# Kernel tuning notes

Measured on AMD Instinct MI355X. Metric: run time of the kernel, lower is better.

The kernel has to match this reference:

```python
import jax, jax.numpy as jnp
import numpy as np

B, S, D = 8, 2048, 768
N_SPANS = 512
MAX_W = 30  # static max span width (inclusive width in tokens)
H = 100
NEG = -1e30


def setup_inputs() -> dict:
    key = jax.random.key(0)
    k1, k2, k3, k4, k5, k6 = jax.random.split(key, 6)
    seq_tensor = jax.random.normal(k1, (B, S, D), dtype=jnp.float32)
    starts = jax.random.randint(k2, (B, N_SPANS), 0, S - MAX_W)
    widths = jax.random.randint(k3, (B, N_SPANS), 1, MAX_W + 1)  # span length in [1, MAX_W]
    ends_excl = starts + widths  # exclusive end, as module expects
    span_indices = jnp.stack([starts, ends_excl], axis=-1).astype(jnp.int64)
    span_mask = (jax.random.uniform(k4, (B, N_SPANS)) > 0.1).astype(jnp.int32)
    att_w = jax.random.normal(k5, (D, 1), dtype=jnp.float32) / np.sqrt(D)
    att_b = jnp.zeros((1,), dtype=jnp.float32)
    ffnn_w = jax.random.normal(k6, (D, H), dtype=jnp.float32) / np.sqrt(D)
    ffnn_b = jnp.zeros((H,), dtype=jnp.float32)
    return {"seq_tensor": seq_tensor, "span_indices": span_indices, "span_mask": span_mask,
            "att_w": att_w, "att_b": att_b, "ffnn_w": ffnn_w, "ffnn_b": ffnn_b}


def reference(seq_tensor, span_indices, span_mask, att_w, att_b, ffnn_w, ffnn_b):
    # exclusive end -> inclusive end (span_end_is_exclusive=True)
    starts = span_indices[..., 0]
    ends = span_indices[..., 1] - 1
    widths = ends - starts  # inclusive width - 1, in [0, MAX_W-1]

    offsets = jnp.arange(MAX_W)  # [W]
    raw_idx = starts[..., None] + offsets  # [B, N, W]
    width_mask = offsets <= widths[..., None]  # [B, N, W]
    idx = jnp.where(width_mask, raw_idx, 0)

    # global attention logits over the sequence: [B, S]
    att_logits = (jnp.einsum('bsd,do->bso', seq_tensor, att_w) + att_b)[..., 0]

    # gather span token embeddings and logits: [B, N, W, D], [B, N, W]
    span_emb = jax.vmap(lambda seq, i: seq[i])(seq_tensor, idx)
    span_logits = jax.vmap(lambda lg, i: lg[i])(att_logits, idx)

    # masked softmax over span width
    span_logits = jnp.where(width_mask, span_logits, NEG)
    attn = jax.nn.softmax(span_logits, axis=-1)  # [B, N, W]

    attended = jnp.einsum('bnw,bnwd->bnd', attn, span_emb)  # [B, N, D]
    attended = attended * span_mask.astype(attended.dtype)[..., None]

    # FeedForward: 1 layer Linear + tanh (dropout=0)
    out = jnp.tanh(jnp.einsum('bnd,dh->bnh', attended, ffnn_w) + ffnn_b)
    return out
```

## Files before the change

### kernel.cpp

```cpp
#include <hip/hip_runtime.h>
#include <cstdint>
#include <cstddef>

#define NB 8
#define NS 2048
#define ND 768
#define NSP 512
#define MAXW 30
#define NH 100
#define LDP 104
#define NKS 24
#define NCF 8
#define BM 16
#define NIT 12

typedef __attribute__((ext_vector_type(8))) short short8;
typedef __attribute__((ext_vector_type(4))) float floatx4;

union U4S8 { uint4 v; short8 s8; unsigned u[4]; unsigned short us[8]; };

__device__ inline unsigned short f2bf(float f) {
    unsigned u = __float_as_uint(f);
    return (unsigned short)((u + 0x7fffu + ((u >> 16) & 1u)) >> 16);
}

__device__ inline void split2(float x0, float x1, unsigned& hi, unsigned& lo) {
    unsigned u0 = __float_as_uint(x0), u1 = __float_as_uint(x1);
    unsigned h0 = u0 & 0xFFFF0000u, h1 = u1 & 0xFFFF0000u;
    hi = (u0 >> 16) | h1;
    float r0 = x0 - __uint_as_float(h0);
    float r1 = x1 - __uint_as_float(h1);
    lo = (__float_as_uint(r0) >> 16) | (__float_as_uint(r1) & 0xFFFF0000u);
}

__global__ __launch_bounds__(256) void pack_b_kernel(
    const float* __restrict__ ffnn_w, const float* __restrict__ att_w,
    uint4* __restrict__ Bfrag)
{
    int ks = blockIdx.x;
    for (int idx = threadIdx.x; idx < NCF * 64; idx += 256) {
        int cf = idx >> 6, lane = idx & 63;
        int q = lane >> 4, r = lane & 15;
        int n = cf * 16 + r;
        U4S8 p;
#pragma unroll
        for (int j = 0; j < 8; j++) {
            int k = ks * 32 + q * 8 + j;
            float v = (n < NH) ? ffnn_w[(size_t)k * NH + n]
                               : (n == NH ? att_w[k] : 0.f);
            p.us[j] = f2bf(v);
        }
        Bfrag[(size_t)(ks * NCF + cf) * 64 + lane] = p.v;
    }
}

__global__ __launch_bounds__(256, 4) void proj_kernel(
    const float* __restrict__ seq, const uint4* __restrict__ Bfrag,
    float* __restrict__ P, float* __restrict__ Lg)
{
    __shared__ unsigned Ahi[BM][36];
    __shared__ unsigned Alo[BM][36];
    const int t = threadIdx.x;
    const int wave = t >> 6, lane = t & 63;
    const int q = lane >> 4, r = lane & 15;
    const int cf0 = wave * 2;
    const int row0 = blockIdx.x * BM;

    floatx4 acc[2] = {{0.f,0.f,0.f,0.f},{0.f,0.f,0.f,0.f}};

    const int sr = t >> 4, sc = t & 15;
    const float4* gA = (const float4*)(seq + (size_t)(row0 + sr) * ND);
    float4 sv = gA[sc];

    const uint4* bp = Bfrag + (size_t)cf0 * 64 + lane;
    uint4 Bc0 = bp[0], Bc1 = bp[64], Bc2 = bp[512], Bc3 = bp[512 + 64];

    for (int i = 0; i < NIT; ++i) {
        unsigned h01, l01, h23, l23;
        split2(sv.x, sv.y, h01, l01);
        split2(sv.z, sv.w, h23, l23);
        __syncthreads();
        { uint2 u; u.x = h01; u.y = h23; *(uint2*)&Ahi[sr][sc * 2] = u; }
        { uint2 u; u.x = l01; u.y = l23; *(uint2*)&Alo[sr][sc * 2] = u; }
        __syncthreads();

        const int ni = (i + 1 < NIT) ? i + 1 : i;
        sv = gA[ni * 16 + sc];
        const size_t nb = (size_t)ni * 1024;
        uint4 Bn0 = bp[nb], Bn1 = bp[nb + 64], Bn2 = bp[nb + 512], Bn3 = bp[nb + 512 + 64];

#pragma unroll
        for (int ksl = 0; ksl < 2; ++ksl) {
            U4S8 ah, al, b0, b1;
            ah.v = *(const uint4*)&Ahi[r][ksl * 16 + q * 4];
            al.v = *(const uint4*)&Alo[r][ksl * 16 + q * 4];
            b0.v = ksl ? Bc2 : Bc0;
            b1.v = ksl ? Bc3 : Bc1;
            acc[0] = __builtin_amdgcn_mfma_f32_16x16x32_bf16(ah.s8, b0.s8, acc[0], 0, 0, 0);
            acc[0] = __builtin_amdgcn_mfma_f32_16x16x32_bf16(al.s8, b0.s8, acc[0], 0, 0, 0);
            acc[1] = __builtin_amdgcn_mfma_f32_16x16x32_bf16(ah.s8, b1.s8, acc[1], 0, 0, 0);
            acc[1] = __builtin_amdgcn_mfma_f32_16x16x32_bf16(al.s8, b1.s8, acc[1], 0, 0, 0);
        }
        Bc0 = Bn0; Bc1 = Bn1; Bc2 = Bn2; Bc3 = Bn3;
    }

#pragma unroll
    for (int c = 0; c < 2; ++c) {
        const int col = (cf0 + c) * 16 + r;
        const int rowb = row0 + q * 4;
        if (col < NH) {
#pragma unroll
            for (int reg = 0; reg < 4; ++reg)
                P[(size_t)(rowb + reg) * LDP + col] = acc[c][reg];
        } else if (col == NH) {
#pragma unroll
            for (int reg = 0; reg < 4; ++reg)
                Lg[rowb + reg] = acc[c][reg];
        }
    }
}

__global__ __launch_bounds__(256, 4) void span_kernel(
    const int* __restrict__ span_idx, const int* __restrict__ span_mask,
    const float* __restrict__ P, const float* __restrict__ Lg,
    const float* __restrict__ ffnn_b, float* __restrict__ out)
{
    const int hw = threadIdx.x >> 5, lane = threadIdx.x & 31;
    const int gs = blockIdx.x * 8 + hw;
    const int b = gs / NSP;
    const int st = span_idx[2 * gs];
    int w = span_idx[2 * gs + 1] - st;
    w = max(1, min(w, MAXW));

    float lg = (lane < w) ? Lg[b * NS + st + lane] : -1e30f;
    float mx = lg;
#pragma unroll
    for (int off = 16; off > 0; off >>= 1) mx = fmaxf(mx, __shfl_xor(mx, off, 32));
    float e = (lane < w) ? __expf(lg - mx) : 0.f;
    float sum = e;
#pragma unroll
    for (int off = 16; off > 0; off >>= 1) sum += __shfl_xor(sum, off, 32);
    float attn = e / sum;

    int cl = min(lane, 24);
    const float4* Pb4 = (const float4*)(P + ((size_t)b * NS + st) * LDP) + cl;
    float4 acc = {0.f, 0.f, 0.f, 0.f};
#pragma unroll
    for (int i = 0; i < MAXW; ++i) {
        float a = __shfl(attn, i, 32);
        if (i < w) {
            float4 v = Pb4[i * (LDP / 4)];
            acc.x += a * v.x; acc.y += a * v.y; acc.z += a * v.z; acc.w += a * v.w;
        }
    }

    if (lane < 25) {
        float m = (float)span_mask[gs];
        float4 bias = ((const float4*)ffnn_b)[lane];
        float4 o;
        o.x = tanhf(m * acc.x + bias.x);
        o.y = tanhf(m * acc.y + bias.y);
        o.z = tanhf(m * acc.z + bias.z);
        o.w = tanhf(m * acc.w + bias.w);
        *(float4*)(out + (size_t)gs * NH + 4 * lane) = o;
    }
}

extern "C" void kernel_launch(void* const* d_in, const int* in_sizes, int n_in,
                              void* d_out, int out_size, void* d_ws, size_t ws_size,
                              hipStream_t stream) {
    const float* seq      = (const float*)d_in[0];
    const int*   span_idx = (const int*)d_in[1];
    const int*   span_msk = (const int*)d_in[2];
    const float* att_w    = (const float*)d_in[3];
    const float* ffnn_w   = (const float*)d_in[5];
    const float* ffnn_b   = (const float*)d_in[6];
    float* out = (float*)d_out;

    char* ws = (char*)d_ws;
    size_t off = 0;
    float* P     = (float*)(ws + off); off += (size_t)NB * NS * LDP * 4;
    uint4* Bfrag = (uint4*)(ws + off); off += (size_t)NKS * NCF * 64 * 16;
    float* Lg    = (float*)(ws + off);

    pack_b_kernel<<<NKS, 256, 0, stream>>>(ffnn_w, att_w, Bfrag);
    proj_kernel<<<(NB * NS) / BM, 256, 0, stream>>>(seq, Bfrag, P, Lg);
    span_kernel<<<(NB * NSP) / 8, 256, 0, stream>>>(span_idx, span_msk, P, Lg, ffnn_b, out);
}
```

Before: 115.5 us.

## Replace per-span softmax gather with prefix sums of exp-weighted projections

Adds a scan kernel that computes prefix sums over the sequence of exp(logit)*P rows plus exp(logit). Each span then needs only two row lookups and a subtraction to form its softmax-weighted average, replacing the 30-row gather and shuffle-based softmax. The projection kernel is also restructured to stage the whole 16x768 A tile in LDS once instead of looping with per-iteration barriers. This drops the max subtraction, so exp of unbounded logits and the differencing of large cumulative sums risk overflow and cancellation error. It also adds an extra launch and a second full-size workspace buffer.

```diff
diff --git a/kernel.cpp b/kernel.cpp
--- a/kernel.cpp
+++ b/kernel.cpp
@@ -11,8 +11,7 @@
 #define LDP 104
 #define NKS 24
 #define NCF 8
-#define BM 16
-#define NIT 12
+#define ASTR 388
 
 typedef __attribute__((ext_vector_type(8))) short short8;
 typedef __attribute__((ext_vector_type(4))) float floatx4;
@@ -54,76 +53,116 @@
     }
 }
 
-__global__ __launch_bounds__(256, 4) void proj_kernel(
+__global__ __launch_bounds__(256, 3) void proj_kernel(
     const float* __restrict__ seq, const uint4* __restrict__ Bfrag,
-    float* __restrict__ P, float* __restrict__ Lg)
-{
-    __shared__ unsigned Ahi[BM][36];
-    __shared__ unsigned Alo[BM][36];
+    float* __restrict__ P)
+{
+    __shared__ unsigned Ahi[16 * ASTR];
+    __shared__ unsigned Alo[16 * ASTR];
     const int t = threadIdx.x;
     const int wave = t >> 6, lane = t & 63;
     const int q = lane >> 4, r = lane & 15;
     const int cf0 = wave * 2;
-    const int row0 = blockIdx.x * BM;
+    const int row0 = blockIdx.x * 16;
+
+    const int tr = t >> 4, tu = t & 15;
+    const float4* gA = (const float4*)(seq + (size_t)(row0 + tr) * ND);
+    float4 v[12];
+#pragma unroll
+    for (int j = 0; j < 12; ++j) v[j] = gA[tu + 16 * j];
+#pragma unroll
+    for (int j = 0; j < 12; ++j) {
+        const int c = tu + 16 * j;
+        unsigned h0, l0, h1, l1;
+        split2(v[j].x, v[j].y, h0, l0);
+        split2(v[j].z, v[j].w, h1, l1);
+        uint2 uh; uh.x = h0; uh.y = h1;
+        uint2 ul; ul.x = l0; ul.y = l1;
+        *(uint2*)&Ahi[tr * ASTR + c * 2] = uh;
+        *(uint2*)&Alo[tr * ASTR + c * 2] = ul;
+    }
+    __syncthreads();
 
     floatx4 acc[2] = {{0.f,0.f,0.f,0.f},{0.f,0.f,0.f,0.f}};
-
-    const int sr = t >> 4, sc = t & 15;
-    const float4* gA = (const float4*)(seq + (size_t)(row0 + sr) * ND);
-    float4 sv = gA[sc];
-
     const uint4* bp = Bfrag + (size_t)cf0 * 64 + lane;
-    uint4 Bc0 = bp[0], Bc1 = bp[64], Bc2 = bp[512], Bc3 = bp[512 + 64];
-
-    for (int i = 0; i < NIT; ++i) {
-        unsigned h01, l01, h23, l23;
-        split2(sv.x, sv.y, h01, l01);
-        split2(sv.z, sv.w, h23, l23);
-        __syncthreads();
-        { uint2 u; u.x = h01; u.y = h23; *(uint2*)&Ahi[sr][sc * 2] = u; }
-        { uint2 u; u.x = l01; u.y = l23; *(uint2*)&Alo[sr][sc * 2] = u; }
-        __syncthreads();
-
-        const int ni = (i + 1 < NIT) ? i + 1 : i;
-        sv = gA[ni * 16 + sc];
-        const size_t nb = (size_t)ni * 1024;
-        uint4 Bn0 = bp[nb], Bn1 = bp[nb + 64], Bn2 = bp[nb + 512], Bn3 = bp[nb + 512 + 64];
-
-#pragma unroll
-        for (int ksl = 0; ksl < 2; ++ksl) {
-            U4S8 ah, al, b0, b1;
-            ah.v = *(const uint4*)&Ahi[r][ksl * 16 + q * 4];
-            al.v = *(const uint4*)&Alo[r][ksl * 16 + q * 4];
-            b0.v = ksl ? Bc2 : Bc0;
-            b1.v = ksl ? Bc3 : Bc1;
-            acc[0] = __builtin_amdgcn_mfma_f32_16x16x32_bf16(ah.s8, b0.s8, acc[0], 0, 0, 0);
-            acc[0] = __builtin_amdgcn_mfma_f32_16x16x32_bf16(al.s8, b0.s8, acc[0], 0, 0, 0);
-            acc[1] = __builtin_amdgcn_mfma_f32_16x16x32_bf16(ah.s8, b1.s8, acc[1], 0, 0, 0);
-            acc[1] = __builtin_amdgcn_mfma_f32_16x16x32_bf16(al.s8, b1.s8, acc[1], 0, 0, 0);
-        }
-        Bc0 = Bn0; Bc1 = Bn1; Bc2 = Bn2; Bc3 = Bn3;
+    uint4 B0 = bp[0], B1 = bp[64];
+
+    for (int ks = 0; ks < NKS; ++ks) {
+        const int nk = (ks + 1 < NKS) ? ks + 1 : ks;
+        uint4 N0 = bp[(size_t)nk * 512], N1 = bp[(size_t)nk * 512 + 64];
+        U4S8 ah, al, b0, b1;
+        ah.v = *(const uint4*)&Ahi[r * ASTR + ks * 16 + q * 4];
+        al.v = *(const uint4*)&Alo[r * ASTR + ks * 16 + q * 4];
+        b0.v = B0; b1.v = B1;
+        acc[0] = __builtin_amdgcn_mfma_f32_16x16x32_bf16(ah.s8, b0.s8, acc[0], 0, 0, 0);
+        acc[0] = __builtin_amdgcn_mfma_f32_16x16x32_bf16(al.s8, b0.s8, acc[0], 0, 0, 0);
+        acc[1] = __builtin_amdgcn_mfma_f32_16x16x32_bf16(ah.s8, b1.s8, acc[1], 0, 0, 0);
+        acc[1] = __builtin_amdgcn_mfma_f32_16x16x32_bf16(al.s8, b1.s8, acc[1], 0, 0, 0);
+        B0 = N0; B1 = N1;
     }
 
 #pragma unroll
     for (int c = 0; c < 2; ++c) {
         const int col = (cf0 + c) * 16 + r;
-        const int rowb = row0 + q * 4;
-        if (col < NH) {
+        if (col <= NH) {
 #pragma unroll
             for (int reg = 0; reg < 4; ++reg)
-                P[(size_t)(rowb + reg) * LDP + col] = acc[c][reg];
-        } else if (col == NH) {
-#pragma unroll
-            for (int reg = 0; reg < 4; ++reg)
-                Lg[rowb + reg] = acc[c][reg];
+                P[(size_t)(row0 + q * 4 + reg) * LDP + col] = acc[c][reg];
         }
     }
 }
 
-__global__ __launch_bounds__(256, 4) void span_kernel(
+__global__ __launch_bounds__(256) void scan_kernel(
+    const float* __restrict__ P, float* __restrict__ CS)
+{
+    __shared__ float4 sm[256];
+    const int b = blockIdx.x / 26, chunk = blockIdx.x % 26;
+    const int t = threadIdx.x;
+    const size_t base = (size_t)b * NS;
+
+    float4 v[8];
+#pragma unroll
+    for (int i = 0; i < 8; ++i) {
+        const int s = t * 8 + i;
+        const float* row = P + (base + s) * LDP;
+        float el = __expf(row[100]);
+        float4 x = *(const float4*)(row + chunk * 4);
+        if (chunk == 25) { x.x = el; x.y = 0.f; x.z = 0.f; x.w = 0.f; }
+        else { x.x *= el; x.y *= el; x.z *= el; x.w *= el; }
+        v[i] = x;
+    }
+#pragma unroll
+    for (int i = 1; i < 8; ++i) {
+        v[i].x += v[i-1].x; v[i].y += v[i-1].y;
+        v[i].z += v[i-1].z; v[i].w += v[i-1].w;
+    }
+    sm[t] = v[7];
+    __syncthreads();
+    for (int off = 1; off < 256; off <<= 1) {
+        float4 add = {0.f,0.f,0.f,0.f};
+        if (t >= off) add = sm[t - off];
+        __syncthreads();
+        if (t >= off) {
+            float4 cur = sm[t];
+            cur.x += add.x; cur.y += add.y; cur.z += add.z; cur.w += add.w;
+            sm[t] = cur;
+        }
+        __syncthreads();
+    }
+    float4 pre = {0.f,0.f,0.f,0.f};
+    if (t > 0) pre = sm[t - 1];
+#pragma unroll
+    for (int i = 0; i < 8; ++i) {
+        float4 o = v[i];
+        o.x += pre.x; o.y += pre.y; o.z += pre.z; o.w += pre.w;
+        ((float4*)CS)[(base + t * 8 + i) * (LDP / 4) + chunk] = o;
+    }
+}
+
+__global__ __launch_bounds__(256) void span_kernel(
     const int* __restrict__ span_idx, const int* __restrict__ span_mask,
-    const float* __restrict__ P, const float* __restrict__ Lg,
-    const float* __restrict__ ffnn_b, float* __restrict__ out)
+    const float* __restrict__ CS, const float* __restrict__ ffnn_b,
+    float* __restrict__ out)
 {
     const int hw = threadIdx.x >> 5, lane = threadIdx.x & 31;
     const int gs = blockIdx.x * 8 + hw;
@@ -132,36 +171,25 @@
     int w = span_idx[2 * gs + 1] - st;
     w = max(1, min(w, MAXW));
 
-    float lg = (lane < w) ? Lg[b * NS + st + lane] : -1e30f;
-    float mx = lg;
-#pragma unroll
-    for (int off = 16; off > 0; off >>= 1) mx = fmaxf(mx, __shfl_xor(mx, off, 32));
-    float e = (lane < w) ? __expf(lg - mx) : 0.f;
-    float sum = e;
-#pragma unroll
-    for (int off = 16; off > 0; off >>= 1) sum += __shfl_xor(sum, off, 32);
-    float attn = e / sum;
-
-    int cl = min(lane, 24);
-    const float4* Pb4 = (const float4*)(P + ((size_t)b * NS + st) * LDP) + cl;
-    float4 acc = {0.f, 0.f, 0.f, 0.f};
-#pragma unroll
-    for (int i = 0; i < MAXW; ++i) {
-        float a = __shfl(attn, i, 32);
-        if (i < w) {
-            float4 v = Pb4[i * (LDP / 4)];
-            acc.x += a * v.x; acc.y += a * v.y; acc.z += a * v.z; acc.w += a * v.w;
-        }
-    }
+    const int cl = min(lane, 25);
+    const float4* cs4 = (const float4*)CS;
+    const size_t rb = (size_t)b * NS;
+    float4 hi = cs4[(rb + st + w - 1) * (LDP / 4) + cl];
+    float4 lo = {0.f, 0.f, 0.f, 0.f};
+    if (st > 0) lo = cs4[(rb + st - 1) * (LDP / 4) + cl];
+
+    float4 d;
+    d.x = hi.x - lo.x; d.y = hi.y - lo.y; d.z = hi.z - lo.z; d.w = hi.w - lo.w;
+    float den = __shfl(d.x, 25, 32);
+    float scale = (float)span_mask[gs] / den;
 
     if (lane < 25) {
-        float m = (float)span_mask[gs];
         float4 bias = ((const float4*)ffnn_b)[lane];
         float4 o;
-        o.x = tanhf(m * acc.x + bias.x);
-        o.y = tanhf(m * acc.y + bias.y);
-        o.z = tanhf(m * acc.z + bias.z);
-        o.w = tanhf(m * acc.w + bias.w);
+        o.x = tanhf(d.x * scale + bias.x);
+        o.y = tanhf(d.y * scale + bias.y);
+        o.z = tanhf(d.z * scale + bias.z);
+        o.w = tanhf(d.w * scale + bias.w);
         *(float4*)(out + (size_t)gs * NH + 4 * lane) = o;
     }
 }
@@ -180,10 +208,11 @@
     char* ws = (char*)d_ws;
     size_t off = 0;
     float* P     = (float*)(ws + off); off += (size_t)NB * NS * LDP * 4;
-    uint4* Bfrag = (uint4*)(ws + off); off += (size_t)NKS * NCF * 64 * 16;
-    float* Lg    = (float*)(ws + off);
+    float* CS    = (float*)(ws + off); off += (size_t)NB * NS * LDP * 4;
+    uint4* Bfrag = (uint4*)(ws + off);
 
     pack_b_kernel<<<NKS, 256, 0, stream>>>(ffnn_w, att_w, Bfrag);
-    proj_kernel<<<(NB * NS) / BM, 256, 0, stream>>>(seq, Bfrag, P, Lg);
-    span_kernel<<<(NB * NSP) / 8, 256, 0, stream>>>(span_idx, span_msk, P, Lg, ffnn_b, out);
-}
+    proj_kernel<<<(NB * NS) / 16, 256, 0, stream>>>(seq, Bfrag, P);
+    scan_kernel<<<NB * (LDP / 4), 256, 0, stream>>>(P, CS);
+    span_kernel<<<(NB * NSP) / 8, 256, 0, stream>>>(span_idx, span_msk, CS, ffnn_b, out);
+}
```

Measured after the change: 122.4 us. +6.0%, slower.
